# Performance work log

Measured on AMD Instinct MI355X. Metric: run time of the kernel, lower is better.

## Reference

```python
import jax, jax.numpy as jnp
import numpy as np

H, B, GH = 4096, 8192, 1024
TEMP = 1.0


def setup_inputs() -> dict:
    key = jax.random.key(0)
    ks = jax.random.split(key, 8)
    return {
        "hidden_states": jax.random.normal(ks[0], (B, H), jnp.float32),
        "attention_mask": jax.random.randint(ks[1], (B,), 0, 2) > 0,
        # similarity_proj: init N(0, 0.02); value_proj: nonzero randoms so kernel math is exercised
        "W_sim": jax.random.normal(ks[2], (H, H), jnp.float32) * 0.02,
        "W_val": jax.random.normal(ks[3], (H, H), jnp.float32) * 0.02,
        # gate_net: Linear(2H, GH) -> GELU -> Linear(GH, H) -> Sigmoid
        "W_g1": jax.random.normal(ks[4], (GH, 2 * H), jnp.float32) * 0.01,
        "b_g1": jnp.zeros((GH,), jnp.float32),
        "W_g2": jax.random.normal(ks[5], (H, GH), jnp.float32) * 0.01,
        "b_g2": jnp.full((H,), -3.0, jnp.float32),
    }


def reference(hidden_states, attention_mask, W_sim, W_val, W_g1, b_g1, W_g2, b_g2):
    b = hidden_states.shape[0]
    # similarity projection + L2 normalize (F.normalize, eps=1e-12)
    proj = hidden_states @ W_sim.T                                  # [B, H]
    norm = jnp.maximum(jnp.linalg.norm(proj, axis=-1, keepdims=True), 1e-12)
    normed = proj / norm
    sim = (normed @ normed.T) / TEMP                                # [B, B]
    # mask self (eye) and invalid samples (columns)
    eye = jnp.eye(b, dtype=bool)
    sim = jnp.where(eye | ~attention_mask[None, :], -jnp.inf, sim)
    weights = jax.nn.softmax(sim, axis=-1)
    weights = jnp.nan_to_num(weights, nan=0.0)
    values = hidden_states @ W_val.T                                # [B, H]
    cross = weights @ values                                        # [B, H]
    # question-aware gate: sigmoid(MLP(cat(h, cross)))
    gate_in = jnp.concatenate([hidden_states, cross], axis=-1)      # [B, 2H]
    h1 = jax.nn.gelu(gate_in @ W_g1.T + b_g1, approximate=False)    # exact GELU (torch default)
    gate = jax.nn.sigmoid(h1 @ W_g2.T + b_g2)                       # [B, H]
    return hidden_states + gate * cross
```

## Files before the change

kernel.cpp:

```cpp
#include <hip/hip_runtime.h>


#define HDIM 4096
#define BATCH 8192
#define GHDIM 1024

typedef unsigned short u16;
typedef short bf16x8 __attribute__((ext_vector_type(8)));
typedef float f32x4 __attribute__((ext_vector_type(4)));

__device__ __forceinline__ u16 f2bf(float f) {
  union { float f; unsigned u; } v; v.f = f;
  unsigned r = v.u + 0x7FFFu + ((v.u >> 16) & 1u);
  return (u16)(r >> 16);
}
__device__ __forceinline__ float bf2f(u16 u) {
  union { unsigned u; float f; } v; v.u = ((unsigned)u) << 16;
  return v.f;
}

__global__ void cast_f32_bf16(const float* __restrict__ src, u16* __restrict__ dst, int n4) {
  int i = blockIdx.x * 256 + threadIdx.x;
  if (i < n4) {
    float4 f = ((const float4*)src)[i];
    ushort4 o;
    o.x = f2bf(f.x); o.y = f2bf(f.y); o.z = f2bf(f.z); o.w = f2bf(f.w);
    ((ushort4*)dst)[i] = o;
  }
}

__global__ void detect_mask(const unsigned char* __restrict__ m, int nbytes, int* __restrict__ flag) {
  __shared__ int cnt[256];
  int c = 0;
  for (int i = threadIdx.x; i < nbytes; i += 256)
    if ((i & 3) && m[i]) c++;
  cnt[threadIdx.x] = c;
  __syncthreads();
  for (int s = 128; s > 0; s >>= 1) {
    if ((int)threadIdx.x < s) cnt[threadIdx.x] += cnt[threadIdx.x + s];
    __syncthreads();
  }
  if (threadIdx.x == 0) *flag = cnt[0];
}

__global__ void compact_mask(const void* __restrict__ raw, const int* __restrict__ flag,
                             int* __restrict__ idxc, int* __restrict__ kinfo) {
  const int t = threadIdx.x;
  const bool isbool = (*flag > 0);
  __shared__ int cnt[256];
  __shared__ int total;
  const int base0 = t * 32;
  int c = 0;
  for (int i = 0; i < 32; i++) {
    int gi = base0 + i;
    int v = isbool ? ((const unsigned char*)raw)[gi] : ((const int*)raw)[gi];
    if (v) c++;
  }
  cnt[t] = c;
  __syncthreads();
  if (t == 0) {
    int acc = 0;
    for (int i = 0; i < 256; i++) { int x = cnt[i]; cnt[i] = acc; acc += x; }
    total = acc;
    kinfo[0] = acc;
    kinfo[1] = (acc + 127) & ~127;
  }
  __syncthreads();
  int w = cnt[t];
  for (int i = 0; i < 32; i++) {
    int gi = base0 + i;
    int v = isbool ? ((const unsigned char*)raw)[gi] : ((const int*)raw)[gi];
    if (v) idxc[w++] = gi;
  }
  for (int i = total + t; i < BATCH; i += 256) idxc[i] = -1;
}

__global__ void gather_rows(const u16* __restrict__ src, u16* __restrict__ dst,
                            const int* __restrict__ idxc, const int* __restrict__ kinfo) {
  int c = blockIdx.x;
  int kc = kinfo[0], kp = kinfo[1];
  if (c >= kp) return;
  uint4* d = (uint4*)(dst + (size_t)c * HDIM);
  if (c < kc) {
    const uint4* s = (const uint4*)(src + (size_t)idxc[c] * HDIM);
    d[threadIdx.x] = s[threadIdx.x];
    d[threadIdx.x + 256] = s[threadIdx.x + 256];
  } else {
    uint4 z = {0, 0, 0, 0};
    d[threadIdx.x] = z;
    d[threadIdx.x + 256] = z;
  }
}

__global__ void normalize_rows(u16* __restrict__ p) {
  int row = blockIdx.x;
  uint4* r = (uint4*)(p + (size_t)row * HDIM);
  uint4 d[2];
  float s = 0.f;
#pragma unroll
  for (int i = 0; i < 2; i++) {
    d[i] = r[i * 256 + threadIdx.x];
    const u16* u = (const u16*)&d[i];
#pragma unroll
    for (int j = 0; j < 8; j++) { float f = bf2f(u[j]); s += f * f; }
  }
  __shared__ float red[256];
  red[threadIdx.x] = s;
  __syncthreads();
  for (int st = 128; st > 0; st >>= 1) {
    if ((int)threadIdx.x < st) red[threadIdx.x] += red[threadIdx.x + st];
    __syncthreads();
  }
  float scale = 1.0f / fmaxf(sqrtf(red[0]), 1e-12f);
#pragma unroll
  for (int i = 0; i < 2; i++) {
    u16* u = (u16*)&d[i];
#pragma unroll
    for (int j = 0; j < 8; j++) u[j] = f2bf(bf2f(u[j]) * scale);
    r[i * 256 + threadIdx.x] = d[i];
  }
}

__global__ void softmax_rows_dyn(u16* __restrict__ sim, const int* __restrict__ kinfo) {
  const int kp = kinfo[1];
  const int row = blockIdx.x;
  uint4* r = (uint4*)(sim + (size_t)row * BATCH);
  float v[32];
  int active[4];
  float mx = -3.0e38f;
#pragma unroll
  for (int ch = 0; ch < 4; ch++) {
    int base = ch * 2048 + threadIdx.x * 8;
    active[ch] = (base < kp);
    if (active[ch]) {
      uint4 d = r[ch * 256 + threadIdx.x];
      const u16* u = (const u16*)&d;
#pragma unroll
      for (int j = 0; j < 8; j++) {
        float f = bf2f(u[j]);
        v[ch * 8 + j] = f;
        mx = fmaxf(mx, f);
      }
    }
  }
  __shared__ float red[256];
  red[threadIdx.x] = mx;
  __syncthreads();
  for (int st = 128; st > 0; st >>= 1) {
    if ((int)threadIdx.x < st) red[threadIdx.x] = fmaxf(red[threadIdx.x], red[threadIdx.x + st]);
    __syncthreads();
  }
  mx = red[0];
  __syncthreads();
  float s = 0.f;
#pragma unroll
  for (int ch = 0; ch < 4; ch++) {
    if (active[ch]) {
#pragma unroll
      for (int j = 0; j < 8; j++) {
        float e = (v[ch * 8 + j] < -1.0e30f) ? 0.f : __expf(v[ch * 8 + j] - mx);
        v[ch * 8 + j] = e;
        s += e;
      }
    }
  }
  red[threadIdx.x] = s;
  __syncthreads();
  for (int st = 128; st > 0; st >>= 1) {
    if ((int)threadIdx.x < st) red[threadIdx.x] += red[threadIdx.x + st];
    __syncthreads();
  }
  float inv = (red[0] > 0.f) ? 1.0f / red[0] : 0.f;
#pragma unroll
  for (int ch = 0; ch < 4; ch++) {
    if (active[ch]) {
      uint4 d;
      u16* u = (u16*)&d;
#pragma unroll
      for (int j = 0; j < 8; j++) u[j] = f2bf(v[ch * 8 + j] * inv);
      r[ch * 256 + threadIdx.x] = d;
    }
  }
}

enum { EPI_BF16 = 0, EPI_SIM = 1, EPI_F32 = 2, EPI_GELU = 3, EPI_FINAL = 4 };

__device__ __forceinline__ void async_load16(const u16* g, u16* l) {
  __builtin_amdgcn_global_load_lds(
      (const __attribute__((address_space(1))) void*)g,
      (__attribute__((address_space(3))) void*)l, 16, 0, 0);
}

template <int EPI>
__global__ __launch_bounds__(256) void gemm_bt(
    const u16* __restrict__ A, int lda,
    const u16* __restrict__ B, int ldb,
    void* __restrict__ C, int ldc,
    int M, int N, int K,
    const int* __restrict__ kinfo, int dynN, int dynK,
    const int* __restrict__ idxc,
    const float* __restrict__ aux,
    const u16* __restrict__ aux2,
    const float* __restrict__ bias) {
  const int rowBase = blockIdx.y * 128;
  const int colBase = blockIdx.x * 128;
  if (dynN && colBase >= kinfo[1]) return;
  const int Keff = dynK ? kinfo[1] : K;

  __shared__ __align__(16) u16 lA[128 * 64];
  __shared__ __align__(16) u16 lB[128 * 64];
  const int tid = threadIdx.x;
  const int lane = tid & 63;
  const int wave = tid >> 6;
  const int waveRow = (wave >> 1) * 64;
  const int waveCol = (wave & 1) * 64;

  const u16* Ab = A + (size_t)rowBase * lda;
  const u16* Bb = B + (size_t)colBase * ldb;

  f32x4 zero = {0.f, 0.f, 0.f, 0.f};
  f32x4 acc[4][4];
#pragma unroll
  for (int mi = 0; mi < 4; mi++)
#pragma unroll
    for (int ni = 0; ni < 4; ni++) acc[mi][ni] = zero;

  for (int kt = 0; kt < Keff; kt += 64) {
#pragma unroll
    for (int i = 0; i < 4; i++) {
      int c = i * 256 + tid;
      int row = c >> 3, k8 = c & 7;
      int gk8 = k8 ^ (row & 7);
      async_load16(Ab + (size_t)row * lda + kt + gk8 * 8, &lA[c * 8]);
    }
#pragma unroll
    for (int i = 0; i < 4; i++) {
      int c = i * 256 + tid;
      int row = c >> 3, k8 = c & 7;
      int gk8 = k8 ^ (row & 7);
      async_load16(Bb + (size_t)row * ldb + kt + gk8 * 8, &lB[c * 8]);
    }
    __syncthreads();
#pragma unroll
    for (int ks = 0; ks < 2; ks++) {
      const int kq = ks * 4 + (lane >> 4);
      bf16x8 af[4], bfr[4];
#pragma unroll
      for (int mi = 0; mi < 4; mi++) {
        int row = waveRow + mi * 16 + (lane & 15);
        af[mi] = *(const bf16x8*)&lA[row * 64 + ((kq ^ (row & 7)) * 8)];
      }
#pragma unroll
      for (int ni = 0; ni < 4; ni++) {
        int row = waveCol + ni * 16 + (lane & 15);
        bfr[ni] = *(const bf16x8*)&lB[row * 64 + ((kq ^ (row & 7)) * 8)];
      }
#pragma unroll
      for (int mi = 0; mi < 4; mi++)
#pragma unroll
        for (int ni = 0; ni < 4; ni++)
          acc[mi][ni] = __builtin_amdgcn_mfma_f32_16x16x32_bf16(af[mi], bfr[ni], acc[mi][ni], 0, 0, 0);
    }
    __syncthreads();
  }

  const int quad = lane >> 4, lcol = lane & 15;
#pragma unroll
  for (int mi = 0; mi < 4; mi++) {
#pragma unroll
    for (int ni = 0; ni < 4; ni++) {
#pragma unroll
      for (int r = 0; r < 4; r++) {
        int grow = rowBase + waveRow + mi * 16 + quad * 4 + r;
        int gcol = colBase + waveCol + ni * 16 + lcol;
        float v = acc[mi][ni][r];
        size_t idx = (size_t)grow * ldc + gcol;
        if constexpr (EPI == EPI_BF16) {
          ((u16*)C)[idx] = f2bf(v);
        } else if constexpr (EPI == EPI_SIM) {
          bool dead = (gcol >= kinfo[0]) || (idxc[gcol] == grow);
          ((u16*)C)[idx] = dead ? (u16)0xFF80 : f2bf(v);
        } else if constexpr (EPI == EPI_F32) {
          ((float*)C)[idx] = v;
        } else if constexpr (EPI == EPI_GELU) {
          float x = v + aux[idx] + bias[gcol];
          float g = 0.5f * x * (1.0f + erff(x * 0.70710678118654752f));
          ((u16*)C)[idx] = f2bf(g);
        } else {
          float x = v + bias[gcol];
          float g = 1.0f / (1.0f + __expf(-x));
          ((float*)C)[idx] = aux[idx] + g * bf2f(aux2[idx]);
        }
      }
    }
  }
}

extern "C" void kernel_launch(void* const* d_in, const int* in_sizes, int n_in,
                              void* d_out, int out_size, void* d_ws, size_t ws_size,
                              hipStream_t stream) {
  const float* hs   = (const float*)d_in[0];
  const void*  mraw = d_in[1];
  const float* Wsim = (const float*)d_in[2];
  const float* Wval = (const float*)d_in[3];
  const float* Wg1  = (const float*)d_in[4];
  const float* bg1  = (const float*)d_in[5];
  const float* Wg2  = (const float*)d_in[6];
  const float* bg2  = (const float*)d_in[7];
  float* out = (float*)d_out;

  char* ws = (char*)d_ws;
  size_t off = 0;
  auto alloc = [&](size_t bytes) {
    char* p = ws + off;
    off += (bytes + 255) & ~(size_t)255;
    return p;
  };
  u16* hidden_bf = (u16*)alloc((size_t)BATCH * HDIM * 2);
  u16* wbuf      = (u16*)alloc((size_t)HDIM * HDIM * 2);
  u16* r1        = (u16*)alloc((size_t)BATCH * HDIM * 2);
  u16* r2        = (u16*)alloc((size_t)BATCH * HDIM * 2);
  int* idxc      = (int*)alloc((size_t)BATCH * 4);
  int* kinfo     = (int*)alloc(256);
  int* flag      = (int*)alloc(256);
  if (off > ws_size) return;

  u16*   simw  = (u16*)d_out;
  float* h1acc = (float*)d_out;
  (void)in_sizes; (void)n_in; (void)out_size;

  dim3 blk(256);

  detect_mask<<<1, 256, 0, stream>>>((const unsigned char*)mraw, BATCH, flag);
  compact_mask<<<1, 256, 0, stream>>>(mraw, flag, idxc, kinfo);

  cast_f32_bf16<<<(BATCH * HDIM / 4) / 256, 256, 0, stream>>>(hs, hidden_bf, BATCH * HDIM / 4);

  cast_f32_bf16<<<(HDIM * HDIM / 4) / 256, 256, 0, stream>>>(Wsim, wbuf, HDIM * HDIM / 4);
  gemm_bt<EPI_BF16><<<dim3(HDIM / 128, BATCH / 128), blk, 0, stream>>>(
      hidden_bf, HDIM, wbuf, HDIM, r1, HDIM, BATCH, HDIM, HDIM,
      nullptr, 0, 0, nullptr, nullptr, nullptr, nullptr);
  normalize_rows<<<BATCH, 256, 0, stream>>>(r1);

  gather_rows<<<BATCH, 256, 0, stream>>>(r1, r2, idxc, kinfo);

  gemm_bt<EPI_SIM><<<dim3(BATCH / 128, BATCH / 128), blk, 0, stream>>>(
      r1, HDIM, r2, HDIM, simw, BATCH, BATCH, BATCH, HDIM,
      kinfo, 1, 0, idxc, nullptr, nullptr, nullptr);
  softmax_rows_dyn<<<BATCH, 256, 0, stream>>>(simw, kinfo);

  gather_rows<<<BATCH, 256, 0, stream>>>(hidden_bf, r1, idxc, kinfo);

  cast_f32_bf16<<<(HDIM * HDIM / 4) / 256, 256, 0, stream>>>(Wval, wbuf, HDIM * HDIM / 4);
  gemm_bt<EPI_BF16><<<dim3(BATCH / 128, HDIM / 128), blk, 0, stream>>>(
      wbuf, HDIM, r1, HDIM, r2, BATCH, HDIM, BATCH, HDIM,
      kinfo, 1, 0, nullptr, nullptr, nullptr, nullptr);

  gemm_bt<EPI_BF16><<<dim3(HDIM / 128, BATCH / 128), blk, 0, stream>>>(
      simw, BATCH, r2, BATCH, r1, HDIM, BATCH, HDIM, BATCH,
      kinfo, 0, 1, nullptr, nullptr, nullptr, nullptr);

  cast_f32_bf16<<<(GHDIM * 2 * HDIM / 4) / 256, 256, 0, stream>>>(Wg1, wbuf, GHDIM * 2 * HDIM / 4);
  gemm_bt<EPI_F32><<<dim3(GHDIM / 128, BATCH / 128), blk, 0, stream>>>(
      hidden_bf, HDIM, wbuf, 2 * HDIM, h1acc, GHDIM, BATCH, GHDIM, HDIM,
      nullptr, 0, 0, nullptr, nullptr, nullptr, nullptr);
  gemm_bt<EPI_GELU><<<dim3(GHDIM / 128, BATCH / 128), blk, 0, stream>>>(
      r1, HDIM, wbuf + HDIM, 2 * HDIM, r2, GHDIM, BATCH, GHDIM, HDIM,
      nullptr, 0, 0, nullptr, h1acc, nullptr, bg1);

  cast_f32_bf16<<<(HDIM * GHDIM / 4) / 256, 256, 0, stream>>>(Wg2, wbuf, HDIM * GHDIM / 4);
  gemm_bt<EPI_FINAL><<<dim3(HDIM / 128, BATCH / 128), blk, 0, stream>>>(
      r2, GHDIM, wbuf, GHDIM, out, HDIM, BATCH, HDIM, GHDIM,
      nullptr, 0, 0, nullptr, hs, r1, bg2);
}
```

Before: 2.029 ms.

## Add 256x256-tile 512-thread GEMM with 4-stage async pipeline and XCD remap

Adds a new GEMM kernel that computes 256x256 output tiles with 8 waves. It uses a 4-slot LDS ring filled by async global-to-LDS loads, split A/B prefetch interleaved with MFMA phases, setprio hints, and a workgroup-id remap that spreads neighbouring tiles across the 8 XCDs. Most of the large GEMMs switch to it. The masked-row padding moves from 128 to 256 to match the larger tile. The aim is more data reuse per tile and better latency hiding, at the cost of higher register and LDS pressure, fewer workgroups, and extra padded work on the dynamic dimensions.

```diff
diff --git a/kernel.cpp b/kernel.cpp
--- a/kernel.cpp
+++ b/kernel.cpp
@@ -63,7 +63,7 @@
     for (int i = 0; i < 256; i++) { int x = cnt[i]; cnt[i] = acc; acc += x; }
     total = acc;
     kinfo[0] = acc;
-    kinfo[1] = (acc + 127) & ~127;
+    kinfo[1] = (acc + 255) & ~255;
   }
   __syncthreads();
   int w = cnt[t];
@@ -189,6 +189,158 @@
   __builtin_amdgcn_global_load_lds(
       (const __attribute__((address_space(1))) void*)g,
       (__attribute__((address_space(3))) void*)l, 16, 0, 0);
+}
+
+template <int EPI>
+__global__ __launch_bounds__(512, 2) void gemm256(
+    const u16* __restrict__ A, int lda,
+    const u16* __restrict__ B, int ldb,
+    void* __restrict__ C, int ldc,
+    int M, int N, int K,
+    const int* __restrict__ kinfo, int dynN, int dynK,
+    const int* __restrict__ idxc,
+    const float* __restrict__ aux,
+    const u16* __restrict__ aux2,
+    const float* __restrict__ bias) {
+  const int nwg = (int)(gridDim.x * gridDim.y);
+  const int orig = (int)(blockIdx.y * gridDim.x + blockIdx.x);
+  int wgid;
+  {
+    int q = nwg >> 3, r = nwg & 7, x = orig & 7, lo = orig >> 3;
+    wgid = (x < r ? x * (q + 1) : r * (q + 1) + (x - r) * q) + lo;
+  }
+  const int bx = wgid % (int)gridDim.x;
+  const int by = wgid / (int)gridDim.x;
+  const int rowBase = by * 256;
+  const int colBase = bx * 256;
+  if (dynN && colBase >= kinfo[1]) return;
+  const int Keff = dynK ? kinfo[1] : K;
+  const int NT = Keff >> 5;
+
+  __shared__ __align__(16) u16 sm[4 * 16384];
+
+  const int tid = threadIdx.x;
+  const int lane = tid & 63, wave = tid >> 6;
+  const int wm = wave >> 2, wn = wave & 3;
+  const int fr = lane & 15, kq = lane >> 4;
+
+  int aOff[8], bOff[4];
+#pragma unroll
+  for (int mi = 0; mi < 8; mi++) {
+    int lin = ((wm * 8 + mi) << 10) + (fr << 6) + (kq << 4);
+    aOff[mi] = lin ^ (((fr >> 3) & 1) << 5);
+  }
+#pragma unroll
+  for (int ni = 0; ni < 4; ni++) {
+    int lin = ((wn * 4 + ni) << 10) + (fr << 6) + (kq << 4);
+    bOff[ni] = (lin ^ (((fr >> 3) & 1) << 5)) + 16384;
+  }
+
+  const int i0row = wave * 16 + (lane >> 2);
+  const int scol = ((lane & 3) << 3) ^ (((lane >> 5) & 1) << 4);
+
+  auto stageA = [&](int tt) {
+    const int sb = (tt & 3) * 16384;
+    const int kt = tt << 5;
+#pragma unroll
+    for (int i = 0; i < 2; i++)
+      async_load16(A + (size_t)(rowBase + i * 128 + i0row) * lda + kt + scol,
+                   sm + sb + i * 4096 + tid * 8);
+  };
+  auto stageB = [&](int tt) {
+    const int sb = (tt & 3) * 16384 + 8192;
+    const int kt = tt << 5;
+#pragma unroll
+    for (int i = 0; i < 2; i++)
+      async_load16(B + (size_t)(colBase + i * 128 + i0row) * ldb + kt + scol,
+                   sm + sb + i * 4096 + tid * 8);
+  };
+
+  f32x4 zero = {0.f, 0.f, 0.f, 0.f};
+  f32x4 acc[8][4];
+#pragma unroll
+  for (int mi = 0; mi < 8; mi++)
+#pragma unroll
+    for (int ni = 0; ni < 4; ni++) acc[mi][ni] = zero;
+
+  if (NT > 0) { stageA(0); stageB(0); }
+  if (NT > 1) { stageA(1); stageB(1); }
+  if (NT > 2) { stageA(2); stageB(2); }
+  if (NT >= 3)      asm volatile("s_waitcnt vmcnt(8)" ::: "memory");
+  else if (NT == 2) asm volatile("s_waitcnt vmcnt(4)" ::: "memory");
+  else              asm volatile("s_waitcnt vmcnt(0)" ::: "memory");
+  __builtin_amdgcn_sched_barrier(0);
+  __builtin_amdgcn_s_barrier();
+
+  for (int t = 0; t < NT; ++t) {
+    const char* slot = (const char*)sm + (size_t)(t & 3) * 32768;
+    const int pt = t + 3;
+    const bool pf = pt < NT;
+
+    bf16x8 af[4], bf[4];
+#pragma unroll
+    for (int mi = 0; mi < 4; mi++) af[mi] = *(const bf16x8*)(slot + aOff[mi]);
+#pragma unroll
+    for (int ni = 0; ni < 4; ni++) bf[ni] = *(const bf16x8*)(slot + bOff[ni]);
+    if (pf) stageA(pt);
+    __builtin_amdgcn_s_barrier();
+    __builtin_amdgcn_s_setprio(1);
+#pragma unroll
+    for (int mi = 0; mi < 4; mi++)
+#pragma unroll
+      for (int ni = 0; ni < 4; ni++)
+        acc[mi][ni] = __builtin_amdgcn_mfma_f32_16x16x32_bf16(af[mi], bf[ni], acc[mi][ni], 0, 0, 0);
+    __builtin_amdgcn_s_setprio(0);
+    __builtin_amdgcn_s_barrier();
+
+#pragma unroll
+    for (int mi = 0; mi < 4; mi++) af[mi] = *(const bf16x8*)(slot + aOff[mi + 4]);
+    if (pf) stageB(pt);
+    __builtin_amdgcn_s_barrier();
+    __builtin_amdgcn_s_setprio(1);
+#pragma unroll
+    for (int mi = 0; mi < 4; mi++)
+#pragma unroll
+      for (int ni = 0; ni < 4; ni++)
+        acc[mi + 4][ni] = __builtin_amdgcn_mfma_f32_16x16x32_bf16(af[mi], bf[ni], acc[mi + 4][ni], 0, 0, 0);
+    __builtin_amdgcn_s_setprio(0);
+    if (pf)                asm volatile("s_waitcnt vmcnt(8)" ::: "memory");
+    else if (t + 2 < NT)   asm volatile("s_waitcnt vmcnt(4)" ::: "memory");
+    else if (t + 1 < NT)   asm volatile("s_waitcnt vmcnt(0)" ::: "memory");
+    __builtin_amdgcn_sched_barrier(0);
+    __builtin_amdgcn_s_barrier();
+  }
+
+  const int quad = lane >> 4, lcol = lane & 15;
+#pragma unroll
+  for (int mi = 0; mi < 8; mi++) {
+#pragma unroll
+    for (int ni = 0; ni < 4; ni++) {
+#pragma unroll
+      for (int r = 0; r < 4; r++) {
+        int grow = rowBase + wm * 128 + mi * 16 + quad * 4 + r;
+        int gcol = colBase + wn * 64 + ni * 16 + lcol;
+        float v = acc[mi][ni][r];
+        size_t idx = (size_t)grow * ldc + gcol;
+        if constexpr (EPI == EPI_BF16) {
+          ((u16*)C)[idx] = f2bf(v);
+        } else if constexpr (EPI == EPI_SIM) {
+          bool dead = (gcol >= kinfo[0]) || (idxc[gcol] == grow);
+          ((u16*)C)[idx] = dead ? (u16)0xFF80 : f2bf(v);
+        } else if constexpr (EPI == EPI_F32) {
+          ((float*)C)[idx] = v;
+        } else if constexpr (EPI == EPI_GELU) {
+          float x = v + aux[idx] + bias[gcol];
+          float g = 0.5f * x * (1.0f + erff(x * 0.70710678118654752f));
+          ((u16*)C)[idx] = f2bf(g);
+        } else {
+          float x = v + bias[gcol];
+          float g = 1.0f / (1.0f + __expf(-x));
+          ((float*)C)[idx] = aux[idx] + g * bf2f(aux2[idx]);
+        }
+      }
+    }
+  }
 }
 
 template <int EPI>
@@ -330,6 +482,7 @@
   (void)in_sizes; (void)n_in; (void)out_size;
 
   dim3 blk(256);
+  dim3 blk5(512);
 
   detect_mask<<<1, 256, 0, stream>>>((const unsigned char*)mraw, BATCH, flag);
   compact_mask<<<1, 256, 0, stream>>>(mraw, flag, idxc, kinfo);
@@ -337,14 +490,14 @@
   cast_f32_bf16<<<(BATCH * HDIM / 4) / 256, 256, 0, stream>>>(hs, hidden_bf, BATCH * HDIM / 4);
 
   cast_f32_bf16<<<(HDIM * HDIM / 4) / 256, 256, 0, stream>>>(Wsim, wbuf, HDIM * HDIM / 4);
-  gemm_bt<EPI_BF16><<<dim3(HDIM / 128, BATCH / 128), blk, 0, stream>>>(
+  gemm256<EPI_BF16><<<dim3(HDIM / 256, BATCH / 256), blk5, 0, stream>>>(
       hidden_bf, HDIM, wbuf, HDIM, r1, HDIM, BATCH, HDIM, HDIM,
       nullptr, 0, 0, nullptr, nullptr, nullptr, nullptr);
   normalize_rows<<<BATCH, 256, 0, stream>>>(r1);
 
   gather_rows<<<BATCH, 256, 0, stream>>>(r1, r2, idxc, kinfo);
 
-  gemm_bt<EPI_SIM><<<dim3(BATCH / 128, BATCH / 128), blk, 0, stream>>>(
+  gemm256<EPI_SIM><<<dim3(BATCH / 256, BATCH / 256), blk5, 0, stream>>>(
       r1, HDIM, r2, HDIM, simw, BATCH, BATCH, BATCH, HDIM,
       kinfo, 1, 0, idxc, nullptr, nullptr, nullptr);
   softmax_rows_dyn<<<BATCH, 256, 0, stream>>>(simw, kinfo);
@@ -352,11 +505,11 @@
   gather_rows<<<BATCH, 256, 0, stream>>>(hidden_bf, r1, idxc, kinfo);
 
   cast_f32_bf16<<<(HDIM * HDIM / 4) / 256, 256, 0, stream>>>(Wval, wbuf, HDIM * HDIM / 4);
-  gemm_bt<EPI_BF16><<<dim3(BATCH / 128, HDIM / 128), blk, 0, stream>>>(
+  gemm256<EPI_BF16><<<dim3(BATCH / 256, HDIM / 256), blk5, 0, stream>>>(
       wbuf, HDIM, r1, HDIM, r2, BATCH, HDIM, BATCH, HDIM,
       kinfo, 1, 0, nullptr, nullptr, nullptr, nullptr);
 
-  gemm_bt<EPI_BF16><<<dim3(HDIM / 128, BATCH / 128), blk, 0, stream>>>(
+  gemm256<EPI_BF16><<<dim3(HDIM / 256, BATCH / 256), blk5, 0, stream>>>(
       simw, BATCH, r2, BATCH, r1, HDIM, BATCH, HDIM, BATCH,
       kinfo, 0, 1, nullptr, nullptr, nullptr, nullptr);
 
@@ -369,7 +522,7 @@
       nullptr, 0, 0, nullptr, h1acc, nullptr, bg1);
 
   cast_f32_bf16<<<(HDIM * GHDIM / 4) / 256, 256, 0, stream>>>(Wg2, wbuf, HDIM * GHDIM / 4);
-  gemm_bt<EPI_FINAL><<<dim3(HDIM / 128, BATCH / 128), blk, 0, stream>>>(
+  gemm256<EPI_FINAL><<<dim3(HDIM / 256, BATCH / 256), blk5, 0, stream>>>(
       r2, GHDIM, wbuf, GHDIM, out, HDIM, BATCH, HDIM, GHDIM,
       nullptr, 0, 0, nullptr, hs, r1, bg2);
 }
```

New measurement: 1.842 ms. 9.2% less time.
